# Optimization experiments

Hardware: AMD Instinct MI355X
Metric: run time of the kernel (lower is better)

## Reference

```python
import jax, jax.numpy as jnp
import numpy as np
import math

B, T, D = 2, 2048, 1024
NH = 16
HD = D // NH


def setup_inputs() -> dict:
    key = jax.random.key(0)
    k1, k2, k3 = jax.random.split(key, 3)
    scale = 0.02
    x = jax.random.normal(k1, (B, T, D), dtype=jnp.float32)
    Wqkv = jax.random.normal(k2, (D, 3 * D), dtype=jnp.float32) * scale
    bqkv = jnp.zeros((3 * D,), dtype=jnp.float32)
    Wproj = jax.random.normal(k3, (D, D), dtype=jnp.float32) * scale
    bproj = jnp.zeros((D,), dtype=jnp.float32)
    return {"x": x, "Wqkv": Wqkv, "bqkv": bqkv, "Wproj": Wproj, "bproj": bproj}


def reference(x, Wqkv, bqkv, Wproj, bproj):
    b, t, c = x.shape
    qkv = x @ Wqkv + bqkv                      # [B,T,3D]
    q, k, v = jnp.split(qkv, 3, axis=2)
    # [B,T,NH,HD] -> [B,NH,T,HD]
    q = q.reshape(b, t, NH, HD).transpose(0, 2, 1, 3)
    k = k.reshape(b, t, NH, HD).transpose(0, 2, 1, 3)
    v = v.reshape(b, t, NH, HD).transpose(0, 2, 1, 3)
    att = jnp.einsum('bhqd,bhkd->bhqk', q, k) / math.sqrt(HD)  # [B,NH,T,T]
    causal = jnp.tril(jnp.ones((t, t), dtype=bool))
    att = jnp.where(causal, att, -jnp.inf)
    att = jax.nn.softmax(att, axis=-1)
    y = jnp.einsum('bhqk,bhkd->bhqd', att, v)  # [B,NH,T,HD]
    y = y.transpose(0, 2, 1, 3).reshape(b, t, c)
    return y @ Wproj + bproj
```

## Files before the change

kernel.cpp:

```cpp
#include <hip/hip_runtime.h>
#include <hip/hip_bf16.h>

#define B_   2
#define T_   2048
#define D_   1024
#define NH_  16
#define HD_  64
#define MROWS (B_*T_)
#define HEADELEMS (B_*NH_*T_*HD_)

#define QSCALE 0.180336880f

typedef unsigned short u16;
typedef unsigned int   u32;

typedef float f32x4  __attribute__((ext_vector_type(4)));
typedef short bf16x8 __attribute__((ext_vector_type(8)));

#define GLP(g, l) __builtin_amdgcn_global_load_lds(                         \
    (const __attribute__((address_space(1))) void*)(g),                     \
    (__attribute__((address_space(3))) void*)(l), 16, 0, 0)

struct Fc { static constexpr bool value = false; };
struct Tc { static constexpr bool value = true;  };

__device__ __forceinline__ u16 f2bf(float f) {
    u32 x = __float_as_uint(f);
    u32 r = (x + 0x7fffu + ((x >> 16) & 1u)) >> 16;
    return (u16)r;
}
__device__ __forceinline__ u32 pkbf2(float a, float b) {
    __hip_bfloat162 h = __float22bfloat162_rn(make_float2(a, b));
    union { __hip_bfloat162 h2; u32 u; } cv; cv.h2 = h; return cv.u;
}

__device__ __forceinline__ void transpose_tile(const float* in, u16* out,
                                               int K, int N, int bx, int by,
                                               int t, float (*Ts)[65])
{
    const int n0 = bx * 64;
    const int k0 = by * 64;
    #pragma unroll
    for (int pass = 0; pass < 4; pass++) {
        const int r = pass * 16 + (t >> 4);
        const int c = (t & 15) * 4;
        float4 v = *(const float4*)(in + (size_t)(k0 + r) * N + n0 + c);
        Ts[r][c] = v.x; Ts[r][c+1] = v.y; Ts[r][c+2] = v.z; Ts[r][c+3] = v.w;
    }
    __syncthreads();
    #pragma unroll
    for (int pass = 0; pass < 2; pass++) {
        const int nn = pass * 32 + (t >> 3);
        const int kk = (t & 7) * 8;
        u16 o[8];
        #pragma unroll
        for (int j = 0; j < 8; j++) o[j] = f2bf(Ts[kk + j][nn]);
        *(uint4*)(out + (size_t)(n0 + nn) * K + k0 + kk) = *(const uint4*)o;
    }
}

__global__ __launch_bounds__(256)
void prep_kernel(const float* __restrict__ x, const float* __restrict__ Wqkv,
                 const float* __restrict__ Wproj, u16* __restrict__ xb,
                 u16* __restrict__ WqkvT, u16* __restrict__ WprojT)
{
    __shared__ float Ts[64][65];
    const int bid = blockIdx.x;
    const int t   = threadIdx.x;
    if (bid < 4096) {
        int i = bid * 256 + t;
        float4 v = ((const float4*)x)[i];
        ushort4 o;
        o.x = f2bf(v.x); o.y = f2bf(v.y); o.z = f2bf(v.z); o.w = f2bf(v.w);
        ((ushort4*)xb)[i] = o;
    } else if (bid < 4096 + 768) {
        int tb = bid - 4096;
        transpose_tile(Wqkv, WqkvT, D_, 3*D_, tb % 48, tb / 48, t, Ts);
    } else {
        int tb = bid - 4864;
        transpose_tile(Wproj, WprojT, D_, D_, tb % 16, tb / 16, t, Ts);
    }
}

__global__ __launch_bounds__(256)
void transpose_conv_kernel(const float* __restrict__ in, u16* __restrict__ out,
                           int K, int N)
{
    __shared__ float Ts[64][65];
    transpose_tile(in, out, K, N, blockIdx.x, blockIdx.y, threadIdx.x, Ts);
}

template <int MODE>
__global__ __launch_bounds__(256)
void gemm_mfma(const u16* __restrict__ A, const u16* __restrict__ BT,
               const float* __restrict__ bias, void* __restrict__ outv,
               int M, int N, int K)
{
    __shared__ u16 As[128][32];
    __shared__ u16 Bs[128][32];

    const int t    = threadIdx.x;
    const int wave = t >> 6;
    const int lane = t & 63;
    const int l16  = lane & 15;
    const int quad = lane >> 4;

    const int m0 = blockIdx.y * 128;
    const int n0 = blockIdx.x * 128;
    const int mb = (wave >> 1) * 64;
    const int nb = (wave & 1) * 64;

    const int r0a  = wave * 16;
    const int r0b  = 64 + wave * 16;
    const int lr_a = r0a + (lane >> 2);
    const int lr_b = r0b + (lane >> 2);
    const int sega = (((lane & 3) ^ ((lr_a >> 1) & 3))) * 8;
    const int segb = (((lane & 3) ^ ((lr_b >> 1) & 3))) * 8;

    const u16* gA0 = A  + (size_t)(m0 + lr_a) * K + sega;
    const u16* gA1 = A  + (size_t)(m0 + lr_b) * K + segb;
    const u16* gB0 = BT + (size_t)(n0 + lr_a) * K + sega;
    const u16* gB1 = BT + (size_t)(n0 + lr_b) * K + segb;

    const int fragoff = (quad ^ ((l16 >> 1) & 3)) * 8;

    const bool swapT = (MODE == 1) && (n0 < 2*D_);

    f32x4 acc[4][4];
    #pragma unroll
    for (int i = 0; i < 4; i++)
        #pragma unroll
        for (int j = 0; j < 4; j++) acc[i][j] = (f32x4){0,0,0,0};

    for (int k0 = 0; k0 < K; k0 += 32) {
        __syncthreads();
        GLP(gA0 + k0, &As[r0a][0]);
        GLP(gA1 + k0, &As[r0b][0]);
        GLP(gB0 + k0, &Bs[r0a][0]);
        GLP(gB1 + k0, &Bs[r0b][0]);
        __syncthreads();

        bf16x8 af[4], bfr[4];
        #pragma unroll
        for (int i = 0; i < 4; i++)
            af[i] = *(const bf16x8*)&As[mb + i*16 + l16][fragoff];
        #pragma unroll
        for (int j = 0; j < 4; j++)
            bfr[j] = *(const bf16x8*)&Bs[nb + j*16 + l16][fragoff];

        if (swapT) {
            #pragma unroll
            for (int p = 0; p < 4; p++)
                #pragma unroll
                for (int q = 0; q < 4; q++)
                    acc[p][q] = __builtin_amdgcn_mfma_f32_16x16x32_bf16(
                        bfr[p], af[q], acc[p][q], 0, 0, 0);
        } else {
            #pragma unroll
            for (int p = 0; p < 4; p++)
                #pragma unroll
                for (int q = 0; q < 4; q++)
                    acc[p][q] = __builtin_amdgcn_mfma_f32_16x16x32_bf16(
                        af[p], bfr[q], acc[p][q], 0, 0, 0);
        }
    }

    const int nsec = n0 + nb;

    if (MODE == 0) {
        #pragma unroll
        for (int q = 0; q < 4; q++) {
            const int n = nsec + q*16 + l16;
            const float bv = bias[n];
            #pragma unroll
            for (int p = 0; p < 4; p++)
                #pragma unroll
                for (int r = 0; r < 4; r++) {
                    const int m = m0 + mb + p*16 + quad*4 + r;
                    ((float*)outv)[(size_t)m * N + n] = acc[p][q][r] + bv;
                }
        }
        return;
    }

    const int sec = nsec >> 10;
    const int dd  = nsec & 1023;
    const int h   = dd >> 6;
    const int bb  = m0 >> 11;
    const size_t hbase = ((size_t)(bb*NH_ + h)) * T_ * HD_;
    u16* out = (u16*)outv;

    if (sec == 2) {
        #pragma unroll
        for (int q = 0; q < 4; q++) {
            const int hd = (q*16 + l16) & 63;
            const float bv = bias[nsec + q*16 + l16];
            u16* rowp = out + (size_t)2 * HEADELEMS + hbase + (size_t)hd * T_;
            #pragma unroll
            for (int p = 0; p < 4; p++) {
                const int tt = (m0 + mb + p*16 + quad*4) & 2047;
                u32 w0 = pkbf2(acc[p][q][0] + bv, acc[p][q][1] + bv);
                u32 w1 = pkbf2(acc[p][q][2] + bv, acc[p][q][3] + bv);
                *(uint2*)(rowp + tt) = make_uint2(w0, w1);
            }
        }
    } else {
        const float sc = (sec == 0) ? QSCALE : 1.0f;
        float4 bv4[4];
        #pragma unroll
        for (int p = 0; p < 4; p++)
            bv4[p] = *(const float4*)(bias + nsec + p*16 + quad*4);

        const int srcA  = l16 + ((quad & 1) << 5);
        const int srcB  = srcA + 16;
        const bool selhi = (quad >> 1) != 0;

        const size_t sbase = (size_t)sec * HEADELEMS + hbase;

        #pragma unroll
        for (int q = 0; q < 4; q++) {
            u32 p01[4], p23[4];
            #pragma unroll
            for (int p = 0; p < 4; p++) {
                float v0 = (acc[p][q][0] + bv4[p].x) * sc;
                float v1 = (acc[p][q][1] + bv4[p].y) * sc;
                float v2 = (acc[p][q][2] + bv4[p].z) * sc;
                float v3 = (acc[p][q][3] + bv4[p].w) * sc;
                p01[p] = pkbf2(v0, v1);
                p23[p] = pkbf2(v2, v3);
            }
            const int tt = (m0 + mb + q*16 + l16) & 2047;
            u16* rowp = out + sbase + (size_t)tt * HD_;
            #pragma unroll
            for (int c = 0; c < 2; c++) {
                u32 t0, t1, r01, r23, r45, r67;
                t0 = (u32)__shfl((int)p01[2*c],   srcA);
                t1 = (u32)__shfl((int)p01[2*c+1], srcA);
                r01 = selhi ? t1 : t0;
                t0 = (u32)__shfl((int)p23[2*c],   srcA);
                t1 = (u32)__shfl((int)p23[2*c+1], srcA);
                r23 = selhi ? t1 : t0;
                t0 = (u32)__shfl((int)p01[2*c],   srcB);
                t1 = (u32)__shfl((int)p01[2*c+1], srcB);
                r45 = selhi ? t1 : t0;
                t0 = (u32)__shfl((int)p23[2*c],   srcB);
                t1 = (u32)__shfl((int)p23[2*c+1], srcB);
                r67 = selhi ? t1 : t0;
                *(uint4*)(rowp + 32*c + quad*8) = make_uint4(r01, r23, r45, r67);
            }
        }
    }
}

__global__ __launch_bounds__(256)
void attn_mfma_kernel(const u16* __restrict__ Q, const u16* __restrict__ K,
                      const u16* __restrict__ VT, u16* __restrict__ y1)
{
    __shared__ u16 Ks[2][64][72];
    __shared__ u16 Vs[2][64][72];

    const int t    = threadIdx.x;
    const int wave = t >> 6;
    const int lane = t & 63;
    const int l16  = lane & 15;
    const int quad = lane >> 4;

    const int hb = blockIdx.x;
    const int yy = blockIdx.y;
    const int a  = yy & 7, g = yy >> 3;
    const int qt = (g == 0) ? 31 - a : (g == 1) ? 16 + a
                 : (g == 2) ? 15 - a : a;
    const int b  = hb >> 4;
    const int h  = hb & 15;
    const size_t base = (size_t)hb * T_ * HD_;

    const int qw0 = qt * 64 + wave * 16;

    bf16x8 qf[2];
    {
        const u16* qp = Q + base + (size_t)(qw0 + l16) * HD_ + quad * 8;
        qf[0] = *(const bf16x8*)(qp);
        qf[1] = *(const bf16x8*)(qp + 32);
    }

    bf16x8 onesf;
    #pragma unroll
    for (int i = 0; i < 8; i++) onesf[i] = (short)0x3F80;

    f32x4 o[4];
    #pragma unroll
    for (int d = 0; d < 4; d++) o[d] = (f32x4){0,0,0,0};
    f32x4 accl = (f32x4){0,0,0,0};

    const int nsteps = qt + 1;

    const int srow = t >> 3;
    const int scol = (t & 7) * 8;

    const int srcA  = l16 + ((quad & 1) << 5);
    const int srcB  = srcA + 16;
    const bool selhi = (quad >> 1) != 0;

    uint4 kr0, kr1, vr0, vr1;
    {
        const u16* kp = K + base + (size_t)srow * HD_ + scol;
        kr0 = *(const uint4*)kp;
        kr1 = *(const uint4*)(kp + 32 * HD_);
        const u16* vp = VT + base + (size_t)srow * T_ + scol;
        vr0 = *(const uint4*)vp;
        vr1 = *(const uint4*)(vp + 32 * T_);
        *(uint4*)&Ks[0][srow][scol]      = kr0;
        *(uint4*)&Ks[0][srow + 32][scol] = kr1;
        *(uint4*)&Vs[0][srow][scol]      = vr0;
        *(uint4*)&Vs[0][srow + 32][scol] = vr1;
    }
    __syncthreads();

    auto compute_tile = [&](int cur, int k0, auto mc) {
        constexpr bool MASKED = decltype(mc)::value;
        f32x4 st[4];
        #pragma unroll
        for (int j = 0; j < 4; j++) {
            bf16x8 kf0 = *(const bf16x8*)&Ks[cur][j*16 + l16][quad * 8];
            bf16x8 kf1 = *(const bf16x8*)&Ks[cur][j*16 + l16][32 + quad * 8];
            f32x4 z = {0,0,0,0};
            z = __builtin_amdgcn_mfma_f32_16x16x32_bf16(kf0, qf[0], z, 0, 0, 0);
            st[j] = __builtin_amdgcn_mfma_f32_16x16x32_bf16(kf1, qf[1], z, 0, 0, 0);
        }

        u32 p01[4], p23[4];
        const int qi = qw0 + l16;
        #pragma unroll
        for (int j = 0; j < 4; j++) {
            const int kb = k0 + j*16 + quad*4;
            float e0 = __builtin_amdgcn_exp2f(st[j][0]);
            float e1 = __builtin_amdgcn_exp2f(st[j][1]);
            float e2 = __builtin_amdgcn_exp2f(st[j][2]);
            float e3 = __builtin_amdgcn_exp2f(st[j][3]);
            if (MASKED) {
                if (kb + 0 > qi) e0 = 0.f;
                if (kb + 1 > qi) e1 = 0.f;
                if (kb + 2 > qi) e2 = 0.f;
                if (kb + 3 > qi) e3 = 0.f;
            }
            p01[j] = pkbf2(e0, e1);
            p23[j] = pkbf2(e2, e3);
        }

        bf16x8 pf[2];
        #pragma unroll
        for (int c = 0; c < 2; c++) {
            u32 t0, t1, r01, r23, r45, r67;
            t0 = (u32)__shfl((int)p01[2*c],   srcA);
            t1 = (u32)__shfl((int)p01[2*c+1], srcA);
            r01 = selhi ? t1 : t0;
            t0 = (u32)__shfl((int)p23[2*c],   srcA);
            t1 = (u32)__shfl((int)p23[2*c+1], srcA);
            r23 = selhi ? t1 : t0;
            t0 = (u32)__shfl((int)p01[2*c],   srcB);
            t1 = (u32)__shfl((int)p01[2*c+1], srcB);
            r45 = selhi ? t1 : t0;
            t0 = (u32)__shfl((int)p23[2*c],   srcB);
            t1 = (u32)__shfl((int)p23[2*c+1], srcB);
            r67 = selhi ? t1 : t0;
            union { u32 u[4]; bf16x8 v; } pk;
            pk.u[0] = r01; pk.u[1] = r23; pk.u[2] = r45; pk.u[3] = r67;
            pf[c] = pk.v;
        }
        accl = __builtin_amdgcn_mfma_f32_16x16x32_bf16(pf[0], onesf, accl, 0, 0, 0);
        accl = __builtin_amdgcn_mfma_f32_16x16x32_bf16(pf[1], onesf, accl, 0, 0, 0);
        #pragma unroll
        for (int d = 0; d < 4; d++) {
            bf16x8 v0 = *(const bf16x8*)&Vs[cur][d*16 + l16][quad * 8];
            bf16x8 v1 = *(const bf16x8*)&Vs[cur][d*16 + l16][32 + quad * 8];
            o[d] = __builtin_amdgcn_mfma_f32_16x16x32_bf16(pf[0], v0, o[d], 0, 0, 0);
            o[d] = __builtin_amdgcn_mfma_f32_16x16x32_bf16(pf[1], v1, o[d], 0, 0, 0);
        }
    };

    for (int kt = 0; kt < nsteps; kt++) {
        const int cur = kt & 1;
        const int k0  = kt * 64;
        const bool have_next = (kt + 1 < nsteps);

        if (have_next) {
            const u16* kp = K + base + (size_t)(k0 + 64 + srow) * HD_ + scol;
            kr0 = *(const uint4*)kp;
            kr1 = *(const uint4*)(kp + 32 * HD_);
            const u16* vp = VT + base + (size_t)srow * T_ + k0 + 64 + scol;
            vr0 = *(const uint4*)vp;
            vr1 = *(const uint4*)(vp + 32 * T_);
        }

        if (kt < qt) compute_tile(cur, k0, Fc{});
        else         compute_tile(cur, k0, Tc{});

        if (have_next) {
            const int nxt = cur ^ 1;
            *(uint4*)&Ks[nxt][srow][scol]      = kr0;
            *(uint4*)&Ks[nxt][srow + 32][scol] = kr1;
            *(uint4*)&Vs[nxt][srow][scol]      = vr0;
            *(uint4*)&Vs[nxt][srow + 32][scol] = vr1;
            __syncthreads();
        }
    }

    #pragma unroll
    for (int r = 0; r < 4; r++) {
        const float inv = 1.f / accl[r];
        const int qi = qw0 + quad*4 + r;
        u16* yp = y1 + ((size_t)(b * T_ + qi)) * D_ + h * HD_ + l16;
        yp[0]  = f2bf(o[0][r] * inv);
        yp[16] = f2bf(o[1][r] * inv);
        yp[32] = f2bf(o[2][r] * inv);
        yp[48] = f2bf(o[3][r] * inv);
    }
}

extern "C" void kernel_launch(void* const* d_in, const int* in_sizes, int n_in,
                              void* d_out, int out_size, void* d_ws, size_t ws_size,
                              hipStream_t stream)
{
    const float* x     = (const float*)d_in[0];
    const float* Wqkv  = (const float*)d_in[1];
    const float* bqkv  = (const float*)d_in[2];
    const float* Wproj = (const float*)d_in[3];
    const float* bproj = (const float*)d_in[4];

    u16* scratch = (u16*)d_out;
    u16* xb      = scratch;
    u16* WqkvT   = scratch + (size_t)MROWS * D_;

    const size_t Y1E = (size_t)MROWS * D_;
    const size_t WPE = (size_t)D_ * D_;

    u16* qkv = (u16*)d_ws;
    u16* Qp  = qkv;
    u16* Kp  = qkv + (size_t)HEADELEMS;
    u16* Vtp = qkv + (size_t)2 * HEADELEMS;

    const bool huge = ws_size >= ((size_t)3 * HEADELEMS + Y1E + WPE) * 2;
    const bool big  = ws_size >= ((size_t)3 * HEADELEMS + Y1E) * 2;

    u16* y1b    = big ? qkv + (size_t)3 * HEADELEMS : scratch;
    u16* y1g    = big ? y1b : Vtp;
    u16* WprojT = huge ? qkv + (size_t)3 * HEADELEMS + Y1E : Kp;

    prep_kernel<<<huge ? 5120 : 4864, 256, 0, stream>>>(
        x, Wqkv, Wproj, xb, WqkvT, WprojT);

    gemm_mfma<1><<<dim3(3*D_/128, MROWS/128), 256, 0, stream>>>(
        xb, WqkvT, bqkv, (void*)qkv, MROWS, 3*D_, D_);

    attn_mfma_kernel<<<dim3(NH_*B_, T_/64), 256, 0, stream>>>(Qp, Kp, Vtp, y1b);

    if (!huge)
        transpose_conv_kernel<<<dim3(D_/64, D_/64), 256, 0, stream>>>(
            Wproj, WprojT, D_, D_);

    if (!big)
        (void)hipMemcpyAsync(y1g, y1b, Y1E * sizeof(u16),
                             hipMemcpyDeviceToDevice, stream);

    gemm_mfma<0><<<dim3(D_/128, MROWS/128), 256, 0, stream>>>(
        y1g, WprojT, bproj, d_out, MROWS, D_, D_);
}
```

Before: 215.9 us.

## Split QKV GEMM into Q/K and V launches, use 64-row tiles for V and proj

The QKV projection becomes two launches. One covers the Q/K columns with 128x128 tiles and the transposed MFMA order; the other covers the V columns with a new 64-row M tile and its own epilogue. The output projection GEMM also moves to 64-row M tiles, doubling its block count to 512 for better CU occupancy on the 1024-wide GEMM. The per-block runtime branch on section is replaced by compile-time modes, at the cost of an extra kernel launch and lower per-block reuse in the smaller tiles.

```diff
diff --git a/kernel.cpp b/kernel.cpp
--- a/kernel.cpp
+++ b/kernel.cpp
@@ -90,13 +90,14 @@
     transpose_tile(in, out, K, N, blockIdx.x, blockIdx.y, threadIdx.x, Ts);
 }
 
-template <int MODE>
+template <int MODE, int MF>
 __global__ __launch_bounds__(256)
 void gemm_mfma(const u16* __restrict__ A, const u16* __restrict__ BT,
                const float* __restrict__ bias, void* __restrict__ outv,
-               int M, int N, int K)
-{
-    __shared__ u16 As[128][32];
+               int M, int N, int K, int n0base)
+{
+    constexpr int MTILE = MF * 32;
+    __shared__ u16 As[MTILE][32];
     __shared__ u16 Bs[128][32];
 
     const int t    = threadIdx.x;
@@ -105,9 +106,9 @@
     const int l16  = lane & 15;
     const int quad = lane >> 4;
 
-    const int m0 = blockIdx.y * 128;
-    const int n0 = blockIdx.x * 128;
-    const int mb = (wave >> 1) * 64;
+    const int m0 = blockIdx.y * MTILE;
+    const int n0 = n0base + blockIdx.x * 128;
+    const int mb = (wave >> 1) * (MF * 16);
     const int nb = (wave & 1) * 64;
 
     const int r0a  = wave * 16;
@@ -124,8 +125,6 @@
 
     const int fragoff = (quad ^ ((l16 >> 1) & 3)) * 8;
 
-    const bool swapT = (MODE == 1) && (n0 < 2*D_);
-
     f32x4 acc[4][4];
     #pragma unroll
     for (int i = 0; i < 4; i++)
@@ -135,29 +134,29 @@
     for (int k0 = 0; k0 < K; k0 += 32) {
         __syncthreads();
         GLP(gA0 + k0, &As[r0a][0]);
-        GLP(gA1 + k0, &As[r0b][0]);
+        if constexpr (MF == 4) GLP(gA1 + k0, &As[r0b][0]);
         GLP(gB0 + k0, &Bs[r0a][0]);
         GLP(gB1 + k0, &Bs[r0b][0]);
         __syncthreads();
 
-        bf16x8 af[4], bfr[4];
-        #pragma unroll
-        for (int i = 0; i < 4; i++)
+        bf16x8 af[MF], bfr[4];
+        #pragma unroll
+        for (int i = 0; i < MF; i++)
             af[i] = *(const bf16x8*)&As[mb + i*16 + l16][fragoff];
         #pragma unroll
         for (int j = 0; j < 4; j++)
             bfr[j] = *(const bf16x8*)&Bs[nb + j*16 + l16][fragoff];
 
-        if (swapT) {
+        if constexpr (MODE == 1) {
             #pragma unroll
             for (int p = 0; p < 4; p++)
                 #pragma unroll
-                for (int q = 0; q < 4; q++)
+                for (int q = 0; q < MF; q++)
                     acc[p][q] = __builtin_amdgcn_mfma_f32_16x16x32_bf16(
                         bfr[p], af[q], acc[p][q], 0, 0, 0);
         } else {
             #pragma unroll
-            for (int p = 0; p < 4; p++)
+            for (int p = 0; p < MF; p++)
                 #pragma unroll
                 for (int q = 0; q < 4; q++)
                     acc[p][q] = __builtin_amdgcn_mfma_f32_16x16x32_bf16(
@@ -167,13 +166,13 @@
 
     const int nsec = n0 + nb;
 
-    if (MODE == 0) {
+    if constexpr (MODE == 0) {
         #pragma unroll
         for (int q = 0; q < 4; q++) {
             const int n = nsec + q*16 + l16;
             const float bv = bias[n];
             #pragma unroll
-            for (int p = 0; p < 4; p++)
+            for (int p = 0; p < MF; p++)
                 #pragma unroll
                 for (int r = 0; r < 4; r++) {
                     const int m = m0 + mb + p*16 + quad*4 + r;
@@ -183,28 +182,30 @@
         return;
     }
 
-    const int sec = nsec >> 10;
     const int dd  = nsec & 1023;
     const int h   = dd >> 6;
     const int bb  = m0 >> 11;
     const size_t hbase = ((size_t)(bb*NH_ + h)) * T_ * HD_;
     u16* out = (u16*)outv;
 
-    if (sec == 2) {
+    if constexpr (MODE == 2) {
         #pragma unroll
         for (int q = 0; q < 4; q++) {
             const int hd = (q*16 + l16) & 63;
             const float bv = bias[nsec + q*16 + l16];
             u16* rowp = out + (size_t)2 * HEADELEMS + hbase + (size_t)hd * T_;
             #pragma unroll
-            for (int p = 0; p < 4; p++) {
+            for (int p = 0; p < MF; p++) {
                 const int tt = (m0 + mb + p*16 + quad*4) & 2047;
                 u32 w0 = pkbf2(acc[p][q][0] + bv, acc[p][q][1] + bv);
                 u32 w1 = pkbf2(acc[p][q][2] + bv, acc[p][q][3] + bv);
                 *(uint2*)(rowp + tt) = make_uint2(w0, w1);
             }
         }
-    } else {
+    }
+
+    if constexpr (MODE == 1) {
+        const int sec = nsec >> 10;
         const float sc = (sec == 0) ? QSCALE : 1.0f;
         float4 bv4[4];
         #pragma unroll
@@ -218,7 +219,7 @@
         const size_t sbase = (size_t)sec * HEADELEMS + hbase;
 
         #pragma unroll
-        for (int q = 0; q < 4; q++) {
+        for (int q = 0; q < MF; q++) {
             u32 p01[4], p23[4];
             #pragma unroll
             for (int p = 0; p < 4; p++) {
@@ -449,8 +450,11 @@
     prep_kernel<<<huge ? 5120 : 4864, 256, 0, stream>>>(
         x, Wqkv, Wproj, xb, WqkvT, WprojT);
 
-    gemm_mfma<1><<<dim3(3*D_/128, MROWS/128), 256, 0, stream>>>(
-        xb, WqkvT, bqkv, (void*)qkv, MROWS, 3*D_, D_);
+    gemm_mfma<1,4><<<dim3(16, MROWS/128), 256, 0, stream>>>(
+        xb, WqkvT, bqkv, (void*)qkv, MROWS, 3*D_, D_, 0);
+
+    gemm_mfma<2,2><<<dim3(8, MROWS/64), 256, 0, stream>>>(
+        xb, WqkvT, bqkv, (void*)qkv, MROWS, 3*D_, D_, 2*D_);
 
     attn_mfma_kernel<<<dim3(NH_*B_, T_/64), 256, 0, stream>>>(Qp, Kp, Vtp, y1b);
 
@@ -462,6 +466,6 @@
         (void)hipMemcpyAsync(y1g, y1b, Y1E * sizeof(u16),
                              hipMemcpyDeviceToDevice, stream);
 
-    gemm_mfma<0><<<dim3(D_/128, MROWS/128), 256, 0, stream>>>(
-        y1g, WprojT, bproj, d_out, MROWS, D_, D_);
-}
+    gemm_mfma<0,2><<<dim3(8, MROWS/64), 256, 0, stream>>>(
+        y1g, WprojT, bproj, d_out, MROWS, D_, D_, 0);
+}
```

Measured after the change: 200.7 us. 1.08x faster.
